# Kernel tuning notes

Hardware: AMD Instinct MI355X
Metric: run time of the kernel (lower is better)

## Reference

```python
import jax, jax.numpy as jnp
import numpy as np

N_NODES = 50000
N_EDGES = 400000


def gat(x, src, dst, W, al, ar, b, n):
    # DGL GATConv: fc -> per-head attention logits -> edge softmax over dst -> weighted sum
    heads, dout = al.shape
    z = (x.reshape(-1, x.shape[-1]) @ W.T).reshape(n, heads, dout)   # [N,H,D]
    el = jnp.sum(z * al, axis=-1)                                    # [N,H]
    er = jnp.sum(z * ar, axis=-1)                                    # [N,H]
    e = jax.nn.leaky_relu(el[src] + er[dst], negative_slope=0.2)     # [E,H]
    emax = jax.ops.segment_max(e, dst, num_segments=n)               # [N,H]
    emax = jnp.where(jnp.isfinite(emax), emax, 0.0)                  # zero-in-degree nodes
    ee = jnp.exp(e - emax[dst])
    den = jax.ops.segment_sum(ee, dst, num_segments=n)               # [N,H]
    alpha = ee / den[dst]                                            # edge softmax
    rst = jax.ops.segment_sum(alpha[:, :, None] * z[src], dst, num_segments=n)  # [N,H,D]
    return rst + b.reshape(heads, dout)


def chain_pass(h, src, dst, n):
    # constrainLayer: m_e = z_src - z_dst, sum at dst, then L2-normalize last dim
    m = jax.ops.segment_sum(h[src] - h[dst], dst, num_segments=n)
    l = jnp.sqrt(jnp.sum(m * m, axis=-1, keepdims=True)) + 1e-7
    return m / l


def setup_inputs() -> dict:
    key = jax.random.key(0)
    ks = jax.random.split(key, 32)
    n, e = N_NODES, N_EDGES
    in_dim, hid, out, H = 64, 128, 64, 4

    def nrm(k, shape, s=0.05):
        return jax.random.normal(k, shape, dtype=jnp.float32) * s

    inp = {
        "x": nrm(ks[0], (n, in_dim), 1.0),
        "src0": jax.random.randint(ks[1], (e,), 0, n, dtype=jnp.int32),
        "dst0": jax.random.randint(ks[2], (e,), 0, n, dtype=jnp.int32),
        "src1": jnp.arange(n - 1, dtype=jnp.int32),
        "dst1": jnp.arange(1, n, dtype=jnp.int32),
        # layer1 (in->hid, 1 head) per etype
        "W1a": nrm(ks[3], (hid, in_dim)), "al1a": nrm(ks[4], (1, hid)), "ar1a": nrm(ks[5], (1, hid)), "b1a": nrm(ks[6], (hid,)),
        "W1b": nrm(ks[7], (hid, in_dim)), "al1b": nrm(ks[8], (1, hid)), "ar1b": nrm(ks[9], (1, hid)), "b1b": nrm(ks[10], (hid,)),
        # layer2 (hid->out, 1 head) per etype
        "W2a": nrm(ks[11], (out, hid)), "al2a": nrm(ks[12], (1, out)), "ar2a": nrm(ks[13], (1, out)), "b2a": nrm(ks[14], (out,)),
        "W2b": nrm(ks[15], (out, hid)), "al2b": nrm(ks[16], (1, out)), "ar2b": nrm(ks[17], (1, out)), "b2b": nrm(ks[18], (out,)),
        # layerMH (out->out, H heads) per etype
        "Wma": nrm(ks[19], (H * out, out)), "alma": nrm(ks[20], (H, out)), "arma": nrm(ks[21], (H, out)), "bma": nrm(ks[22], (H * out,)),
        "Wmb": nrm(ks[23], (H * out, out)), "almb": nrm(ks[24], (H, out)), "armb": nrm(ks[25], (H, out)), "bmb": nrm(ks[26], (H * out,)),
        "r": jax.random.uniform(ks[27], (1,), dtype=jnp.float32),
    }
    return inp


def reference(x, src0, dst0, src1, dst1,
              W1a, al1a, ar1a, b1a, W1b, al1b, ar1b, b1b,
              W2a, al2a, ar2a, b2a, W2b, al2b, ar2b, b2b,
              Wma, alma, arma, bma, Wmb, almb, armb, bmb, r):
    n = x.shape[0]
    # HeteroGraphConv(mean) over etypes {interacts, chain}
    h = 0.5 * (gat(x, src0, dst0, W1a, al1a, ar1a, b1a, n)
               + gat(x, src1, dst1, W1b, al1b, ar1b, b1b, n))          # [N,1,hid]
    h = 0.5 * (gat(h, src0, dst0, W2a, al2a, ar2a, b2a, n)
               + gat(h, src1, dst1, W2b, al2b, ar2b, b2b, n))          # [N,1,out]
    radius = jnp.clip(r, 0.01, 3.0)  # computed but unused (dead code in original)
    dh = chain_pass(h, src1, dst1, n)                                   # [N,1,out]
    conh = jnp.cumsum(dh, axis=-2)  # cumsum over singleton head axis (as in original)
    hm = 0.5 * (gat(conh, src0, dst0, Wma, alma, arma, bma, n)
                + gat(conh, src1, dst1, Wmb, almb, armb, bmb, n))       # [N,H,out]
    # per-head chain pass + cumsum over nodes, vectorized across heads
    ds = chain_pass(hm, src1, dst1, n)                                  # [N,H,out]
    res = jnp.cumsum(ds, axis=0)                                        # torch cumsum dim=-2 of [N,out] per head
    return res
```

## Files before the change

kernel.cpp:

```cpp
#include <hip/hip_runtime.h>
#include <math.h>

__device__ __forceinline__ float wred_sum(float v){
  #pragma unroll
  for (int o = 32; o > 0; o >>= 1) v += __shfl_xor(v, o);
  return v;
}
__device__ __forceinline__ float wred_max(float v){
  #pragma unroll
  for (int o = 32; o > 0; o >>= 1) v = fmaxf(v, __shfl_xor(v, o));
  return v;
}
__device__ __forceinline__ float lrelu(float v){ return v > 0.f ? v : 0.2f * v; }

__global__ void k_hist(const int* __restrict__ dst, int* __restrict__ deg, int E){
  int t = blockIdx.x * blockDim.x + threadIdx.x;
  if (t < E) atomicAdd(&deg[dst[t]], 1);
}

__global__ void k_deg_bsum(const int* __restrict__ deg, int* __restrict__ bsum, int n){
  __shared__ int s[256];
  int b = blockIdx.x, t = threadIdx.x;
  int i = b * 256 + t;
  s[t] = (i < n) ? deg[i] : 0;
  __syncthreads();
  for (int o = 128; o > 0; o >>= 1){ if (t < o) s[t] += s[t + o]; __syncthreads(); }
  if (t == 0) bsum[b] = s[0];
}
__global__ void k_bsum_scan(int* __restrict__ bsum, int nblk){
  __shared__ int s[256];
  int t = threadIdx.x;
  s[t] = (t < nblk) ? bsum[t] : 0;
  __syncthreads();
  for (int o = 1; o < 256; o <<= 1){
    int add = (t >= o) ? s[t - o] : 0;
    __syncthreads();
    s[t] += add;
    __syncthreads();
  }
  if (t < nblk) bsum[t] = (t > 0) ? s[t - 1] : 0;
}
__global__ void k_rowptr(const int* __restrict__ deg, const int* __restrict__ bsum,
                         int* __restrict__ rowptr, int* __restrict__ cursor, int n, int E){
  __shared__ int s[256];
  int b = blockIdx.x, t = threadIdx.x;
  int i = b * 256 + t;
  int v = (i < n) ? deg[i] : 0;
  s[t] = v;
  __syncthreads();
  for (int o = 1; o < 256; o <<= 1){
    int add = (t >= o) ? s[t - o] : 0;
    __syncthreads();
    s[t] += add;
    __syncthreads();
  }
  if (i < n){
    int rp = bsum[b] + s[t] - v;
    rowptr[i] = rp;
    cursor[i] = rp;
    if (i == n - 1) rowptr[n] = E;
  }
}

__global__ void k_scatter(const int* __restrict__ src, const int* __restrict__ dst,
                          int* __restrict__ cursor, int* __restrict__ esrc, int E){
  int t = blockIdx.x * blockDim.x + threadIdx.x;
  if (t < E){
    int d = dst[t];
    int p = atomicAdd(&cursor[d], 1);
    esrc[p] = src[t];
  }
}

__global__ void k_valvar_all(const float* __restrict__ W1, const float* __restrict__ al1, const float* __restrict__ ar1,
                             const float* __restrict__ W2, const float* __restrict__ al2, const float* __restrict__ ar2,
                             const float* __restrict__ Wm, const float* __restrict__ alm, const float* __restrict__ arm,
                             float* __restrict__ vv1, float* __restrict__ vv2, float* __restrict__ vvm){
  int b = blockIdx.x, k = threadIdx.x;
  if (b == 0){
    if (k < 64){
      float v = 0.f, w = 0.f;
      for (int c = 0; c < 128; c++){ float ww = W1[c * 64 + k]; v += al1[c] * ww; w += ar1[c] * ww; }
      vv1[k] = v; vv1[64 + k] = w;
    }
  } else if (b == 1){
    float v = 0.f, w = 0.f;
    for (int c = 0; c < 64; c++){ float ww = W2[c * 128 + k]; v += al2[c] * ww; w += ar2[c] * ww; }
    vv2[k] = v; vv2[128 + k] = w;
  } else {
    if (k < 64){
      for (int h = 0; h < 4; h++){
        float v = 0.f, w = 0.f;
        for (int c = 0; c < 64; c++){
          float ww = Wm[(size_t)(h * 64 + c) * 64 + k];
          v += alm[h * 64 + c] * ww; w += arm[h * 64 + c] * ww;
        }
        vvm[(2 * h) * 64 + k] = v; vvm[(2 * h + 1) * 64 + k] = w;
      }
    }
  }
}

template<int K, int C, int H>
__global__ void k_gemm2(const float* __restrict__ x,
                        const float* __restrict__ Wa, const float* __restrict__ Wb,
                        const float* __restrict__ vv,
                        float* __restrict__ za, float* __restrict__ zb,
                        float* __restrict__ el, float* __restrict__ er, int n){
  constexpr int K4 = K / 4, NKC = K / 64, NCC = C / 64;
  constexpr int ROWS = 16384 / (K * 4);
  constexpr int RPW = ROWS / 4;
  constexpr int NP = NCC;
  __shared__ float  XS[ROWS][K];
  __shared__ float4 WQ[2][16 * 65];

  int t = threadIdx.x, lane = t & 63, wv = t >> 6;
  int rowbase = blockIdx.x * ROWS;

  for (int idx = t; idx < ROWS * K4; idx += 256){
    int r = idx / K4, k4 = idx - r * K4;
    int row = rowbase + r;
    float4 v = make_float4(0.f, 0.f, 0.f, 0.f);
    if (row < n) v = *(const float4*)&x[(size_t)row * K + k4 * 4];
    *(float4*)&XS[r][k4 * 4] = v;
  }

  const int r0 = wv * RPW;
  float acc0[RPW], acc1[RPW];

  for (int p = 0; p < NP; p++){
    int q0 = 2 * p, q1 = q0 + 1;
    const float* Wp0 = (q0 < NCC) ? (Wa + (size_t)q0 * 64 * K) : (Wb + (size_t)(q0 - NCC) * 64 * K);
    const float* Wp1 = (q1 < NCC) ? (Wa + (size_t)q1 * 64 * K) : (Wb + (size_t)(q1 - NCC) * 64 * K);
    #pragma unroll
    for (int r = 0; r < RPW; r++){ acc0[r] = 0.f; acc1[r] = 0.f; }

    for (int kc = 0; kc < NKC; kc++){
      __syncthreads();
      const float4* A4 = (const float4*)Wp0;
      const float4* B4 = (const float4*)Wp1;
      for (int idx = t; idx < 1024; idx += 256){
        int c = idx >> 4, k4 = idx & 15;
        WQ[0][k4 * 65 + c] = A4[(size_t)c * K4 + kc * 16 + k4];
        WQ[1][k4 * 65 + c] = B4[(size_t)c * K4 + kc * 16 + k4];
      }
      __syncthreads();
      #pragma unroll 4
      for (int k4 = 0; k4 < 16; k4++){
        float4 w0 = WQ[0][k4 * 65 + lane];
        float4 w1 = WQ[1][k4 * 65 + lane];
        #pragma unroll
        for (int r = 0; r < RPW; r++){
          float4 xk = *(const float4*)&XS[r0 + r][kc * 64 + k4 * 4];
          acc0[r] += xk.x * w0.x + xk.y * w0.y + xk.z * w0.z + xk.w * w0.w;
          acc1[r] += xk.x * w1.x + xk.y * w1.y + xk.z * w1.z + xk.w * w1.w;
        }
      }
    }

    float* z0 = (q0 < NCC) ? za : zb;
    float* z1 = (q1 < NCC) ? za : zb;
    int c0 = ((q0 < NCC) ? q0 : q0 - NCC) * 64;
    int c1 = ((q1 < NCC) ? q1 : q1 - NCC) * 64;
    #pragma unroll
    for (int r = 0; r < RPW; r++){
      int row = rowbase + r0 + r;
      if (row < n){
        z0[(size_t)row * C + c0 + lane] = acc0[r];
        z1[(size_t)row * C + c1 + lane] = acc1[r];
      }
    }
  }

  {
    #pragma unroll
    for (int r = 0; r < RPW; r++) acc0[r] = 0.f;
    for (int kc = 0; kc < NKC; kc++){
      __syncthreads();
      const float4* V4 = (const float4*)vv;
      for (int idx = t; idx < 2 * H * 16; idx += 256){
        int c = idx >> 4, k4 = idx & 15;
        WQ[0][k4 * 65 + c] = V4[(size_t)c * K4 + kc * 16 + k4];
      }
      __syncthreads();
      #pragma unroll 4
      for (int k4 = 0; k4 < 16; k4++){
        float4 w0 = WQ[0][k4 * 65 + lane];
        #pragma unroll
        for (int r = 0; r < RPW; r++){
          float4 xk = *(const float4*)&XS[r0 + r][kc * 64 + k4 * 4];
          acc0[r] += xk.x * w0.x + xk.y * w0.y + xk.z * w0.z + xk.w * w0.w;
        }
      }
    }
    if (lane < 2 * H){
      int h = lane >> 1;
      float* dst = (lane & 1) ? er : el;
      #pragma unroll
      for (int r = 0; r < RPW; r++){
        int row = rowbase + r0 + r;
        if (row < n) dst[(size_t)row * H + h] = acc0[r];
      }
    }
  }
}

template<int D>
__global__ void k_gat_h1(const int* __restrict__ rowptr, const int* __restrict__ esrc,
                         const float* __restrict__ z, const float* __restrict__ el,
                         const float* __restrict__ er, const float* __restrict__ b,
                         const float* __restrict__ zb, const float* __restrict__ bb,
                         float* __restrict__ out, int n){
  constexpr int DR = D / 64;
  int lane = threadIdx.x & 63;
  int i = blockIdx.x * (blockDim.x >> 6) + (threadIdx.x >> 6);
  if (i >= n) return;
  int s0 = rowptr[i], s1 = rowptr[i + 1];
  float eri = er[i];
  float m = -INFINITY;
  for (int e = s0 + lane; e < s1; e += 64)
    m = fmaxf(m, lrelu(el[esrc[e]] + eri));
  m = wred_max(m);
  float den = 0.f, den2 = 0.f;
  float acc[DR], acc2[DR];
  #pragma unroll
  for (int j = 0; j < DR; j++){ acc[j] = 0.f; acc2[j] = 0.f; }
  int e = s0;
  for (; e + 1 < s1; e += 2){
    int sA = esrc[e], sB = esrc[e + 1];
    float wA = __expf(lrelu(el[sA] + eri) - m);
    float wB = __expf(lrelu(el[sB] + eri) - m);
    den += wA; den2 += wB;
    const float* zA = z + (size_t)sA * D;
    const float* zB = z + (size_t)sB * D;
    #pragma unroll
    for (int j = 0; j < DR; j++){
      acc[j]  += wA * zA[j * 64 + lane];
      acc2[j] += wB * zB[j * 64 + lane];
    }
  }
  if (e < s1){
    int sA = esrc[e];
    float wA = __expf(lrelu(el[sA] + eri) - m);
    den += wA;
    const float* zA = z + (size_t)sA * D;
    #pragma unroll
    for (int j = 0; j < DR; j++) acc[j] += wA * zA[j * 64 + lane];
  }
  den += den2;
  float inv = (s1 > s0) ? 1.f / den : 0.f;
  float* op = out + (size_t)i * D;
  #pragma unroll
  for (int j = 0; j < DR; j++){
    int c = j * 64 + lane;
    float chain = bb[c];
    if (i > 0) chain += zb[(size_t)(i - 1) * D + c];
    op[c] = 0.5f * (((acc[j] + acc2[j]) * inv + b[c]) + chain);
  }
}

__global__ void k_gat_mh(const int* __restrict__ rowptr, const int* __restrict__ esrc,
                         const float* __restrict__ z, const float* __restrict__ el,
                         const float* __restrict__ er, const float* __restrict__ b,
                         const float* __restrict__ zb, const float* __restrict__ bb,
                         float* __restrict__ out, int n){
  int lane = threadIdx.x & 63;
  int i = blockIdx.x * (blockDim.x >> 6) + (threadIdx.x >> 6);
  if (i >= n) return;
  int s0 = rowptr[i], s1 = rowptr[i + 1];
  const float4 eri = *(const float4*)(er + (size_t)i * 4);
  float m0 = -INFINITY, m1 = -INFINITY, m2 = -INFINITY, m3 = -INFINITY;
  for (int e = s0 + lane; e < s1; e += 64){
    float4 e4 = *(const float4*)(el + (size_t)esrc[e] * 4);
    m0 = fmaxf(m0, lrelu(e4.x + eri.x));
    m1 = fmaxf(m1, lrelu(e4.y + eri.y));
    m2 = fmaxf(m2, lrelu(e4.z + eri.z));
    m3 = fmaxf(m3, lrelu(e4.w + eri.w));
  }
  m0 = wred_max(m0); m1 = wred_max(m1); m2 = wred_max(m2); m3 = wred_max(m3);
  float d0 = 0.f, d1 = 0.f, d2 = 0.f, d3 = 0.f;
  float a0 = 0.f, a1 = 0.f, a2 = 0.f, a3 = 0.f;
  float d0B = 0.f, d1B = 0.f, d2B = 0.f, d3B = 0.f;
  float a0B = 0.f, a1B = 0.f, a2B = 0.f, a3B = 0.f;
  int e = s0;
  for (; e + 1 < s1; e += 2){
    int sA = esrc[e], sB = esrc[e + 1];
    float4 eA = *(const float4*)(el + (size_t)sA * 4);
    float4 eB = *(const float4*)(el + (size_t)sB * 4);
    const float* zA = z + (size_t)sA * 256;
    const float* zB = z + (size_t)sB * 256;
    float w0 = __expf(lrelu(eA.x + eri.x) - m0);
    float w1 = __expf(lrelu(eA.y + eri.y) - m1);
    float w2 = __expf(lrelu(eA.z + eri.z) - m2);
    float w3 = __expf(lrelu(eA.w + eri.w) - m3);
    float v0 = __expf(lrelu(eB.x + eri.x) - m0);
    float v1 = __expf(lrelu(eB.y + eri.y) - m1);
    float v2 = __expf(lrelu(eB.z + eri.z) - m2);
    float v3 = __expf(lrelu(eB.w + eri.w) - m3);
    d0 += w0; d1 += w1; d2 += w2; d3 += w3;
    d0B += v0; d1B += v1; d2B += v2; d3B += v3;
    a0 += w0 * zA[lane];        a0B += v0 * zB[lane];
    a1 += w1 * zA[64 + lane];   a1B += v1 * zB[64 + lane];
    a2 += w2 * zA[128 + lane];  a2B += v2 * zB[128 + lane];
    a3 += w3 * zA[192 + lane];  a3B += v3 * zB[192 + lane];
  }
  if (e < s1){
    int sA = esrc[e];
    float4 eA = *(const float4*)(el + (size_t)sA * 4);
    const float* zA = z + (size_t)sA * 256;
    float w0 = __expf(lrelu(eA.x + eri.x) - m0);
    float w1 = __expf(lrelu(eA.y + eri.y) - m1);
    float w2 = __expf(lrelu(eA.z + eri.z) - m2);
    float w3 = __expf(lrelu(eA.w + eri.w) - m3);
    d0 += w0; d1 += w1; d2 += w2; d3 += w3;
    a0 += w0 * zA[lane];
    a1 += w1 * zA[64 + lane];
    a2 += w2 * zA[128 + lane];
    a3 += w3 * zA[192 + lane];
  }
  d0 += d0B; d1 += d1B; d2 += d2B; d3 += d3B;
  a0 += a0B; a1 += a1B; a2 += a2B; a3 += a3B;
  float has = (s1 > s0) ? 1.f : 0.f;
  a0 = (has != 0.f) ? a0 / d0 : 0.f;
  a1 = (has != 0.f) ? a1 / d1 : 0.f;
  a2 = (has != 0.f) ? a2 / d2 : 0.f;
  a3 = (has != 0.f) ? a3 / d3 : 0.f;
  float* op = out + (size_t)i * 256;
  float av[4] = {a0, a1, a2, a3};
  #pragma unroll
  for (int h = 0; h < 4; h++){
    int c = h * 64 + lane;
    float chain = bb[c];
    if (i > 0) chain += zb[(size_t)(i - 1) * 256 + c];
    op[c] = 0.5f * ((av[h] + b[c]) + chain);
  }
}

__global__ void k_chainpass64(const float* __restrict__ h, float* __restrict__ dh, int n){
  int lane = threadIdx.x & 63;
  int i = blockIdx.x * (blockDim.x >> 6) + (threadIdx.x >> 6);
  if (i >= n) return;
  float d = 0.f;
  if (i > 0) d = h[(size_t)(i - 1) * 64 + lane] - h[(size_t)i * 64 + lane];
  float ss = wred_sum(d * d);
  dh[(size_t)i * 64 + lane] = d / (sqrtf(ss) + 1e-7f);
}

__global__ void k_chainpass_mh(const float* __restrict__ hm, float* __restrict__ ds, int n){
  int lane = threadIdx.x & 63;
  int i = blockIdx.x * (blockDim.x >> 6) + (threadIdx.x >> 6);
  if (i >= n) return;
  const float* cur = hm + (size_t)i * 256;
  const float* prv = hm + (size_t)(i - 1) * 256;
  #pragma unroll
  for (int h = 0; h < 4; h++){
    int c = h * 64 + lane;
    float d = (i > 0) ? (prv[c] - cur[c]) : 0.f;
    float ss = wred_sum(d * d);
    ds[(size_t)i * 256 + c] = d / (sqrtf(ss) + 1e-7f);
  }
}

__global__ void k_chunk_sum(const float* __restrict__ ds, float* __restrict__ csum, int n, int ch){
  int b = blockIdx.x, t = threadIdx.x;
  int r0 = b * ch, r1 = r0 + ch; if (r1 > n) r1 = n;
  float s = 0.f;
  for (int r = r0; r < r1; r++) s += ds[(size_t)r * 256 + t];
  csum[(size_t)b * 256 + t] = s;
}
__global__ void k_scan_chunks_par(float* __restrict__ csum, int nb){
  __shared__ float s[512];
  int col = blockIdx.x;
  int t = threadIdx.x;
  s[t] = (t < nb) ? csum[(size_t)t * 256 + col] : 0.f;
  __syncthreads();
  #pragma unroll
  for (int o = 1; o < 512; o <<= 1){
    float add = (t >= o) ? s[t - o] : 0.f;
    __syncthreads();
    s[t] += add;
    __syncthreads();
  }
  if (t < nb) csum[(size_t)t * 256 + col] = (t > 0) ? s[t - 1] : 0.f;
}
__global__ void k_apply_scan(float* __restrict__ ds, const float* __restrict__ csum, int n, int ch){
  int b = blockIdx.x, t = threadIdx.x;
  int r0 = b * ch, r1 = r0 + ch; if (r1 > n) r1 = n;
  float run = csum[(size_t)b * 256 + t];
  for (int r = r0; r < r1; r++){
    run += ds[(size_t)r * 256 + t];
    ds[(size_t)r * 256 + t] = run;
  }
}

extern "C" void kernel_launch(void* const* d_in, const int* in_sizes, int n_in,
                              void* d_out, int out_size, void* d_ws, size_t ws_size,
                              hipStream_t stream){
  const float* x    = (const float*)d_in[0];
  const int*   src0 = (const int*)d_in[1];
  const int*   dst0 = (const int*)d_in[2];
  const float* W1a  = (const float*)d_in[5];
  const float* al1a = (const float*)d_in[6];
  const float* ar1a = (const float*)d_in[7];
  const float* b1a  = (const float*)d_in[8];
  const float* W1b  = (const float*)d_in[9];
  const float* b1b  = (const float*)d_in[12];
  const float* W2a  = (const float*)d_in[13];
  const float* al2a = (const float*)d_in[14];
  const float* ar2a = (const float*)d_in[15];
  const float* b2a  = (const float*)d_in[16];
  const float* W2b  = (const float*)d_in[17];
  const float* b2b  = (const float*)d_in[20];
  const float* Wma  = (const float*)d_in[21];
  const float* alma = (const float*)d_in[22];
  const float* arma = (const float*)d_in[23];
  const float* bma  = (const float*)d_in[24];
  const float* Wmb  = (const float*)d_in[25];
  const float* bmb  = (const float*)d_in[28];

  const int n = in_sizes[0] / 64;
  const int E = in_sizes[1];
  const size_t nf = (size_t)n;

  float* ws  = (float*)d_ws;
  float* A   = ws;
  float* B   = A + nf * 256;
  float* C   = B + nf * 256;
  float* D2  = C + nf * 256;
  float* E2  = D2 + nf * 64;
  float* ela = E2 + nf * 64;
  float* era = ela + nf * 4;
  const int ch = 100;
  const int nb = (n + ch - 1) / ch;
  float* csum = era + nf * 4;
  int* deg    = (int*)(csum + (size_t)nb * 256);
  int* rowptr = deg + n;
  int* cursor = rowptr + (n + 1);
  int* esrc   = cursor + n;
  int* bsum   = esrc + E;
  float* vv1  = (float*)(bsum + 256);
  float* vv2  = vv1 + 128;
  float* vvm  = vv2 + 256;

  float* dsout = (float*)d_out;

  const int nwb  = (n + 3) / 4;
  const int eb   = (E + 255) / 256;
  const int nblk = (n + 255) / 256;

  hipMemsetAsync(deg, 0, (size_t)n * sizeof(int), stream);
  k_hist<<<eb, 256, 0, stream>>>(dst0, deg, E);
  k_deg_bsum<<<nblk, 256, 0, stream>>>(deg, bsum, n);
  k_bsum_scan<<<1, 256, 0, stream>>>(bsum, nblk);
  k_rowptr<<<nblk, 256, 0, stream>>>(deg, bsum, rowptr, cursor, n, E);
  k_scatter<<<eb, 256, 0, stream>>>(src0, dst0, cursor, esrc, E);

  k_valvar_all<<<3, 128, 0, stream>>>(W1a, al1a, ar1a, W2a, al2a, ar2a, Wma, alma, arma,
                                      vv1, vv2, vvm);

  k_gemm2<64, 128, 1><<<(n + 63) / 64, 256, 0, stream>>>(x, W1a, W1b, vv1, A, B, ela, era, n);
  k_gat_h1<128><<<nwb, 256, 0, stream>>>(rowptr, esrc, A, ela, era, b1a, B, b1b, C, n);

  k_gemm2<128, 64, 1><<<(n + 31) / 32, 256, 0, stream>>>(C, W2a, W2b, vv2, A, B, ela, era, n);
  k_gat_h1<64><<<nwb, 256, 0, stream>>>(rowptr, esrc, A, ela, era, b2a, B, b2b, D2, n);

  k_chainpass64<<<nwb, 256, 0, stream>>>(D2, E2, n);

  k_gemm2<64, 256, 4><<<(n + 63) / 64, 256, 0, stream>>>(E2, Wma, Wmb, vvm, A, B, ela, era, n);
  k_gat_mh<<<nwb, 256, 0, stream>>>(rowptr, esrc, A, ela, era, bma, B, bmb, C, n);

  k_chainpass_mh<<<nwb, 256, 0, stream>>>(C, dsout, n);

  k_chunk_sum<<<nb, 256, 0, stream>>>(dsout, csum, n, ch);
  k_scan_chunks_par<<<256, 512, 0, stream>>>(csum, nb);
  k_apply_scan<<<nb, 256, 0, stream>>>(dsout, csum, n, ch);
}
```

Measured before the change: 698.4 us.

## Vectorize GAT aggregation with float4 gathers and split edges across sub-wavefronts

The single-head GAT aggregation kernel now assigns D/4 lanes per edge with float4 loads, so one wavefront processes several edges at once, and a cross-lane shuffle reduction combines the partial sums. The multi-head kernel switches to one float4 per lane covering 4 contiguous columns, with each lane computing only its own head's softmax weight. The goal is fewer, wider memory transactions and more edges in flight per wavefront for the irregular z gathers. In exchange there is extra shuffle-reduction work, per-lane head selection logic, and masked lanes on partial edge batches.

```diff
diff --git a/kernel.cpp b/kernel.cpp
--- a/kernel.cpp
+++ b/kernel.cpp
@@ -12,6 +12,9 @@
   return v;
 }
 __device__ __forceinline__ float lrelu(float v){ return v > 0.f ? v : 0.2f * v; }
+__device__ __forceinline__ float sel4(int h, float4 v){
+  return (h & 2) ? ((h & 1) ? v.w : v.z) : ((h & 1) ? v.y : v.x);
+}
 
 __global__ void k_hist(const int* __restrict__ dst, int* __restrict__ deg, int E){
   int t = blockIdx.x * blockDim.x + threadIdx.x;
@@ -211,8 +214,10 @@
                          const float* __restrict__ er, const float* __restrict__ b,
                          const float* __restrict__ zb, const float* __restrict__ bb,
                          float* __restrict__ out, int n){
-  constexpr int DR = D / 64;
+  constexpr int LPS = D / 4;
+  constexpr int NS  = 64 / LPS;
   int lane = threadIdx.x & 63;
+  int q = lane / LPS, j = lane % LPS;
   int i = blockIdx.x * (blockDim.x >> 6) + (threadIdx.x >> 6);
   if (i >= n) return;
   int s0 = rowptr[i], s1 = rowptr[i + 1];
@@ -221,41 +226,39 @@
   for (int e = s0 + lane; e < s1; e += 64)
     m = fmaxf(m, lrelu(el[esrc[e]] + eri));
   m = wred_max(m);
-  float den = 0.f, den2 = 0.f;
-  float acc[DR], acc2[DR];
+  float4 acc = make_float4(0.f, 0.f, 0.f, 0.f);
+  float den = 0.f;
+  for (int base = s0; base < s1; base += NS){
+    int e = base + q;
+    bool ok = (e < s1);
+    int s = esrc[ok ? e : s0];
+    float w = ok ? __expf(lrelu(el[s] + eri) - m) : 0.f;
+    den += w;
+    float4 zv = *(const float4*)&z[(size_t)s * D + 4 * j];
+    acc.x += w * zv.x; acc.y += w * zv.y; acc.z += w * zv.z; acc.w += w * zv.w;
+  }
   #pragma unroll
-  for (int j = 0; j < DR; j++){ acc[j] = 0.f; acc2[j] = 0.f; }
-  int e = s0;
-  for (; e + 1 < s1; e += 2){
-    int sA = esrc[e], sB = esrc[e + 1];
-    float wA = __expf(lrelu(el[sA] + eri) - m);
-    float wB = __expf(lrelu(el[sB] + eri) - m);
-    den += wA; den2 += wB;
-    const float* zA = z + (size_t)sA * D;
-    const float* zB = z + (size_t)sB * D;
-    #pragma unroll
-    for (int j = 0; j < DR; j++){
-      acc[j]  += wA * zA[j * 64 + lane];
-      acc2[j] += wB * zB[j * 64 + lane];
-    }
-  }
-  if (e < s1){
-    int sA = esrc[e];
-    float wA = __expf(lrelu(el[sA] + eri) - m);
-    den += wA;
-    const float* zA = z + (size_t)sA * D;
-    #pragma unroll
-    for (int j = 0; j < DR; j++) acc[j] += wA * zA[j * 64 + lane];
-  }
-  den += den2;
+  for (int o = LPS; o < 64; o <<= 1){
+    acc.x += __shfl_xor(acc.x, o);
+    acc.y += __shfl_xor(acc.y, o);
+    acc.z += __shfl_xor(acc.z, o);
+    acc.w += __shfl_xor(acc.w, o);
+    den   += __shfl_xor(den, o);
+  }
   float inv = (s1 > s0) ? 1.f / den : 0.f;
-  float* op = out + (size_t)i * D;
-  #pragma unroll
-  for (int j = 0; j < DR; j++){
-    int c = j * 64 + lane;
-    float chain = bb[c];
-    if (i > 0) chain += zb[(size_t)(i - 1) * D + c];
-    op[c] = 0.5f * (((acc[j] + acc2[j]) * inv + b[c]) + chain);
+  if (lane < LPS){
+    float4 bv  = *(const float4*)&b[4 * j];
+    float4 ch  = *(const float4*)&bb[4 * j];
+    if (i > 0){
+      float4 zbv = *(const float4*)&zb[(size_t)(i - 1) * D + 4 * j];
+      ch.x += zbv.x; ch.y += zbv.y; ch.z += zbv.z; ch.w += zbv.w;
+    }
+    float4 o4;
+    o4.x = 0.5f * ((acc.x * inv + bv.x) + ch.x);
+    o4.y = 0.5f * ((acc.y * inv + bv.y) + ch.y);
+    o4.z = 0.5f * ((acc.z * inv + bv.z) + ch.z);
+    o4.w = 0.5f * ((acc.w * inv + bv.w) + ch.w);
+    *(float4*)&out[(size_t)i * D + 4 * j] = o4;
   }
 }
 
@@ -265,75 +268,63 @@
                          const float* __restrict__ zb, const float* __restrict__ bb,
                          float* __restrict__ out, int n){
   int lane = threadIdx.x & 63;
+  int h = lane >> 4;
   int i = blockIdx.x * (blockDim.x >> 6) + (threadIdx.x >> 6);
   if (i >= n) return;
   int s0 = rowptr[i], s1 = rowptr[i + 1];
-  const float4 eri = *(const float4*)(er + (size_t)i * 4);
+  const float4 eri4 = *(const float4*)(er + (size_t)i * 4);
   float m0 = -INFINITY, m1 = -INFINITY, m2 = -INFINITY, m3 = -INFINITY;
   for (int e = s0 + lane; e < s1; e += 64){
     float4 e4 = *(const float4*)(el + (size_t)esrc[e] * 4);
-    m0 = fmaxf(m0, lrelu(e4.x + eri.x));
-    m1 = fmaxf(m1, lrelu(e4.y + eri.y));
-    m2 = fmaxf(m2, lrelu(e4.z + eri.z));
-    m3 = fmaxf(m3, lrelu(e4.w + eri.w));
+    m0 = fmaxf(m0, lrelu(e4.x + eri4.x));
+    m1 = fmaxf(m1, lrelu(e4.y + eri4.y));
+    m2 = fmaxf(m2, lrelu(e4.z + eri4.z));
+    m3 = fmaxf(m3, lrelu(e4.w + eri4.w));
   }
   m0 = wred_max(m0); m1 = wred_max(m1); m2 = wred_max(m2); m3 = wred_max(m3);
-  float d0 = 0.f, d1 = 0.f, d2 = 0.f, d3 = 0.f;
-  float a0 = 0.f, a1 = 0.f, a2 = 0.f, a3 = 0.f;
-  float d0B = 0.f, d1B = 0.f, d2B = 0.f, d3B = 0.f;
-  float a0B = 0.f, a1B = 0.f, a2B = 0.f, a3B = 0.f;
+  float msel = (h & 2) ? ((h & 1) ? m3 : m2) : ((h & 1) ? m1 : m0);
+  float erh  = sel4(h, eri4);
+
+  float4 acc  = make_float4(0.f, 0.f, 0.f, 0.f);
+  float4 accB = make_float4(0.f, 0.f, 0.f, 0.f);
+  float den = 0.f, denB = 0.f;
   int e = s0;
   for (; e + 1 < s1; e += 2){
     int sA = esrc[e], sB = esrc[e + 1];
     float4 eA = *(const float4*)(el + (size_t)sA * 4);
     float4 eB = *(const float4*)(el + (size_t)sB * 4);
-    const float* zA = z + (size_t)sA * 256;
-    const float* zB = z + (size_t)sB * 256;
-    float w0 = __expf(lrelu(eA.x + eri.x) - m0);
-    float w1 = __expf(lrelu(eA.y + eri.y) - m1);
-    float w2 = __expf(lrelu(eA.z + eri.z) - m2);
-    float w3 = __expf(lrelu(eA.w + eri.w) - m3);
-    float v0 = __expf(lrelu(eB.x + eri.x) - m0);
-    float v1 = __expf(lrelu(eB.y + eri.y) - m1);
-    float v2 = __expf(lrelu(eB.z + eri.z) - m2);
-    float v3 = __expf(lrelu(eB.w + eri.w) - m3);
-    d0 += w0; d1 += w1; d2 += w2; d3 += w3;
-    d0B += v0; d1B += v1; d2B += v2; d3B += v3;
-    a0 += w0 * zA[lane];        a0B += v0 * zB[lane];
-    a1 += w1 * zA[64 + lane];   a1B += v1 * zB[64 + lane];
-    a2 += w2 * zA[128 + lane];  a2B += v2 * zB[128 + lane];
-    a3 += w3 * zA[192 + lane];  a3B += v3 * zB[192 + lane];
+    float wA = __expf(lrelu(sel4(h, eA) + erh) - msel);
+    float wB = __expf(lrelu(sel4(h, eB) + erh) - msel);
+    den += wA; denB += wB;
+    float4 zA = *(const float4*)&z[(size_t)sA * 256 + 4 * lane];
+    float4 zB = *(const float4*)&z[(size_t)sB * 256 + 4 * lane];
+    acc.x  += wA * zA.x; acc.y  += wA * zA.y; acc.z  += wA * zA.z; acc.w  += wA * zA.w;
+    accB.x += wB * zB.x; accB.y += wB * zB.y; accB.z += wB * zB.z; accB.w += wB * zB.w;
   }
   if (e < s1){
     int sA = esrc[e];
     float4 eA = *(const float4*)(el + (size_t)sA * 4);
-    const float* zA = z + (size_t)sA * 256;
-    float w0 = __expf(lrelu(eA.x + eri.x) - m0);
-    float w1 = __expf(lrelu(eA.y + eri.y) - m1);
-    float w2 = __expf(lrelu(eA.z + eri.z) - m2);
-    float w3 = __expf(lrelu(eA.w + eri.w) - m3);
-    d0 += w0; d1 += w1; d2 += w2; d3 += w3;
-    a0 += w0 * zA[lane];
-    a1 += w1 * zA[64 + lane];
-    a2 += w2 * zA[128 + lane];
-    a3 += w3 * zA[192 + lane];
-  }
-  d0 += d0B; d1 += d1B; d2 += d2B; d3 += d3B;
-  a0 += a0B; a1 += a1B; a2 += a2B; a3 += a3B;
-  float has = (s1 > s0) ? 1.f : 0.f;
-  a0 = (has != 0.f) ? a0 / d0 : 0.f;
-  a1 = (has != 0.f) ? a1 / d1 : 0.f;
-  a2 = (has != 0.f) ? a2 / d2 : 0.f;
-  a3 = (has != 0.f) ? a3 / d3 : 0.f;
-  float* op = out + (size_t)i * 256;
-  float av[4] = {a0, a1, a2, a3};
-  #pragma unroll
-  for (int h = 0; h < 4; h++){
-    int c = h * 64 + lane;
-    float chain = bb[c];
-    if (i > 0) chain += zb[(size_t)(i - 1) * 256 + c];
-    op[c] = 0.5f * ((av[h] + b[c]) + chain);
-  }
+    float wA = __expf(lrelu(sel4(h, eA) + erh) - msel);
+    den += wA;
+    float4 zA = *(const float4*)&z[(size_t)sA * 256 + 4 * lane];
+    acc.x += wA * zA.x; acc.y += wA * zA.y; acc.z += wA * zA.z; acc.w += wA * zA.w;
+  }
+  den += denB;
+  acc.x += accB.x; acc.y += accB.y; acc.z += accB.z; acc.w += accB.w;
+  float inv = (s1 > s0) ? 1.f / den : 0.f;
+
+  float4 bv = *(const float4*)&b[4 * lane];
+  float4 ch = *(const float4*)&bb[4 * lane];
+  if (i > 0){
+    float4 zbv = *(const float4*)&zb[(size_t)(i - 1) * 256 + 4 * lane];
+    ch.x += zbv.x; ch.y += zbv.y; ch.z += zbv.z; ch.w += zbv.w;
+  }
+  float4 o4;
+  o4.x = 0.5f * ((acc.x * inv + bv.x) + ch.x);
+  o4.y = 0.5f * ((acc.y * inv + bv.y) + ch.y);
+  o4.z = 0.5f * ((acc.z * inv + bv.z) + ch.z);
+  o4.w = 0.5f * ((acc.w * inv + bv.w) + ch.w);
+  *(float4*)&out[(size_t)i * 256 + 4 * lane] = o4;
 }
 
 __global__ void k_chainpass64(const float* __restrict__ h, float* __restrict__ dh, int n){
```

Result: no change. 692.2 us (-0.9%).
